# Performance work log

Measured on AMD Instinct MI355X. Metric: run time of the kernel, lower is better.

The kernel has to match this reference:

```python
import jax, jax.numpy as jnp
import numpy as np

BS, Q, NCLS, T = 16, 900, 1000, 100  # batch, queries, classes, targets per image
W_CLASS, W_BBOX, W_GIOU = 1.0, 1.0, 1.0


def _lsa_min(cost):
    """Jonker-Volgenant shortest-augmenting-path assignment (minimization).
    cost: [n, m] with n <= m. Returns (rows=arange(n), cols) matching
    scipy.optimize.linear_sum_assignment."""
    cost = np.asarray(cost, dtype=np.float64)
    n, m = cost.shape
    INF = np.inf
    u = np.zeros(n + 1)
    v = np.zeros(m + 1)
    p = np.zeros(m + 1, dtype=np.int64)   # p[j] = row (1-indexed) assigned to col j
    way = np.zeros(m + 1, dtype=np.int64)
    for i in range(1, n + 1):
        p[0] = i
        j0 = 0
        minv = np.full(m + 1, INF)
        used = np.zeros(m + 1, dtype=bool)
        while True:
            used[j0] = True
            i0 = p[j0]
            cur = cost[i0 - 1] - u[i0] - v[1:]
            free = ~used[1:]
            upd = free & (cur < minv[1:])
            minv[1:] = np.where(upd, cur, minv[1:])
            way[1:] = np.where(upd, j0, way[1:])
            free_idx = np.nonzero(free)[0]
            j1 = free_idx[np.argmin(minv[1:][free_idx])] + 1
            delta = minv[j1]
            used_idx = np.nonzero(used)[0]
            u[p[used_idx]] += delta
            v[used_idx] -= delta
            minv[1:][free] -= delta
            j0 = j1
            if p[j0] == 0:
                break
        while j0 != 0:
            j1 = way[j0]
            p[j0] = p[j1]
            j0 = j1
    cols = np.empty(n, dtype=np.int64)
    for j in range(1, m + 1):
        if p[j] > 0:
            cols[p[j] - 1] = j - 1
    return np.arange(n, dtype=np.int64), cols


def setup_inputs() -> dict:
    key = jax.random.key(0)
    k1, k2, k3, k4 = jax.random.split(key, 4)
    return {
        "pred_logits": jax.random.normal(k1, (BS, Q, NCLS), dtype=jnp.float32),
        "pred_boxes": jax.random.uniform(k2, (BS, Q, 4), dtype=jnp.float32),
        "tgt_ids": jax.random.randint(k3, (BS * T,), 0, NCLS, dtype=jnp.int64),
        "tgt_bbox": jax.random.uniform(k4, (BS * T, 4), dtype=jnp.float32),
    }


def _cost_matrix(pred_logits, pred_boxes, tgt_ids, tgt_bbox):
    out_prob = jax.nn.softmax(pred_logits.reshape(BS * Q, NCLS), axis=-1)
    out_bbox = pred_boxes.reshape(BS * Q, 4)
    cost_class = -out_prob[:, tgt_ids]                                   # [BS*Q, BS*T]
    cost_bbox = jnp.sum(jnp.abs(out_bbox[:, None, :] - tgt_bbox[None, :, :]), axis=-1)  # L1 cdist
    # cost_giou is zeros_like(cost_bbox) in the source, so its term vanishes
    Cm = W_BBOX * cost_bbox + W_CLASS * cost_class
    return Cm.reshape(BS, Q, BS * T)


def reference(pred_logits, pred_boxes, tgt_ids, tgt_bbox):
    Cm = _cost_matrix(pred_logits, pred_boxes, tgt_ids, tgt_bbox)
    Cnp = np.asarray(jax.device_get(Cm))
    idx_i, idx_j = [], []
    for b in range(BS):
        block = Cnp[b, :, b * T:(b + 1) * T]          # [Q, T], Q > T
        r, c = _lsa_min(block.T)                      # solve transpose: rows=targets, cols=preds
        order = np.argsort(c)                         # scipy sorts by prediction index
        idx_i.append(c[order])                        # selected prediction indices
        idx_j.append(r[order])                        # corresponding target indices
    return Cm, jnp.asarray(np.stack(idx_i)), jnp.asarray(np.stack(idx_j))
```

## Files before the change

### kernel.cpp

```cpp
#include <hip/hip_runtime.h>
#include <hip/hip_bf16.h>
#include <math.h>

#define BS   16
#define NQ   900
#define NCLS 1000
#define NT   100
#define MQ   900
#define NCOL (BS * NT)
#define NSLOT 15

typedef float f32x4 __attribute__((ext_vector_type(4)));

#define WAVE_FENCE() asm volatile("" ::: "memory")

__device__ __forceinline__ unsigned umin32(unsigned a, unsigned b) {
  return a < b ? a : b;
}

template <int CTRL>
__device__ __forceinline__ unsigned dpp_min_u32(unsigned x) {
  const unsigned o = (unsigned)__builtin_amdgcn_update_dpp(
      (int)x, (int)x, CTRL, 0xF, 0xF, false);
  return o < x ? o : x;
}

__device__ __forceinline__ unsigned wave_min_u32(unsigned x) {
  x = dpp_min_u32<0xB1>(x);
  x = dpp_min_u32<0x4E>(x);
  x = dpp_min_u32<0x114>(x);
  x = dpp_min_u32<0x118>(x);
  x = dpp_min_u32<0x142>(x);
  x = dpp_min_u32<0x143>(x);
  return (unsigned)__builtin_amdgcn_readlane((int)x, 63);
}

__device__ __forceinline__ unsigned f32key(float f) {
  unsigned e = __float_as_uint(f);
  return (e & 0x80000000u) ? ~e : (e | 0x80000000u);
}
__device__ __forceinline__ float f32unkey(unsigned k) {
  return __uint_as_float((k & 0x80000000u) ? (k ^ 0x80000000u) : ~k);
}

__global__ __launch_bounds__(256) void statcost_kernel(
    const float* __restrict__ logits, const float* __restrict__ boxes,
    const int* __restrict__ ids, const float* __restrict__ tbox,
    float* __restrict__ stats, float* __restrict__ costT, int id_stride) {
  const int tid = threadIdx.x, w = tid >> 6, lane = tid & 63;
  const int row = blockIdx.x * 4 + w;
  const int b = row / NQ;
  const int q = row - b * NQ;

  __shared__ float lbuf[4][NCLS];
  float* lr = lbuf[w];

  const float4* l4 = (const float4*)(logits + (size_t)row * NCLS);
  float4 vv[4];
  float lmax = -INFINITY;
#pragma unroll
  for (int it = 0; it < 4; ++it) {
    const int idx = it * 64 + lane;
    if (idx < NCLS / 4) {
      vv[it] = l4[idx];
      ((float4*)lr)[idx] = vv[it];
      lmax = fmaxf(lmax,
                   fmaxf(fmaxf(vv[it].x, vv[it].y), fmaxf(vv[it].z, vv[it].w)));
    }
  }
  for (int o = 32; o > 0; o >>= 1) lmax = fmaxf(lmax, __shfl_xor(lmax, o, 64));
  float psum = 0.f;
#pragma unroll
  for (int it = 0; it < 4; ++it) {
    const int idx = it * 64 + lane;
    if (idx < NCLS / 4) {
      psum += __expf(vv[it].x - lmax) + __expf(vv[it].y - lmax) +
              __expf(vv[it].z - lmax) + __expf(vv[it].w - lmax);
    }
  }
  for (int o = 32; o > 0; o >>= 1) psum += __shfl_xor(psum, o, 64);
  if (lane == 0) { stats[2 * row] = lmax; stats[2 * row + 1] = psum; }

  const float4 bb = *reinterpret_cast<const float4*>(boxes + (size_t)row * 4);
  const float inv = 1.f / psum;
  for (int rr = lane; rr < NT; rr += 64) {
    const int j = b * NT + rr;
    const int id = ids[(size_t)j * id_stride];
    const float4 tb = *reinterpret_cast<const float4*>(tbox + (size_t)j * 4);
    float d = fabsf(bb.x - tb.x);
    d += fabsf(bb.y - tb.y);
    d += fabsf(bb.z - tb.z);
    d += fabsf(bb.w - tb.w);
    costT[((size_t)b * NT + rr) * MQ + q] = d - __expf(lr[id] - lmax) * inv;
  }
}

__global__ __launch_bounds__(64) void rowmin_kernel(
    const float* __restrict__ costT, float* __restrict__ u_w,
    int* __restrict__ amin_w) {
  const int bid = blockIdx.x;
  const float* rowp = costT + (size_t)bid * MQ;
  const int lane = threadIdx.x;
  const unsigned UMAX = 0xFFFFFFFFu;

  unsigned tv[NSLOT];
#pragma unroll
  for (int s = 0; s < NSLOT; ++s) {
    const int c = s * 64 + lane;
    tv[s] = (c < MQ) ? f32key(rowp[c]) : UMAX;
  }
  unsigned m[NSLOT];
#pragma unroll
  for (int s = 0; s < NSLOT; ++s) m[s] = tv[s];
#pragma unroll
  for (int st = 1; st < NSLOT; st <<= 1) {
#pragma unroll
    for (int s = 0; s + st < NSLOT; s += 2 * st) m[s] = umin32(m[s], m[s + st]);
  }
  const unsigned s_vb = wave_min_u32(m[0]);
  unsigned cj[NSLOT];
#pragma unroll
  for (int s = 0; s < NSLOT; ++s)
    cj[s] = (tv[s] == s_vb) ? (unsigned)(s * 64 + lane) : UMAX;
#pragma unroll
  for (int st = 1; st < NSLOT; st <<= 1) {
#pragma unroll
    for (int s = 0; s + st < NSLOT; s += 2 * st)
      cj[s] = umin32(cj[s], cj[s + st]);
  }
  const unsigned s_j = wave_min_u32(cj[0]);
  if (lane == 0) { u_w[bid] = f32unkey(s_vb); amin_w[bid] = (int)s_j; }
}

__global__ __launch_bounds__(256) void main_kernel(
    const float* __restrict__ logits, const float* __restrict__ boxes,
    const int* __restrict__ ids, const float* __restrict__ tbox,
    const float* __restrict__ stats, const float* __restrict__ costT,
    const float* __restrict__ u_w, const int* __restrict__ amin_w,
    float* __restrict__ C, float* __restrict__ out_i,
    float* __restrict__ out_j, int id_stride) {
  __shared__ float lbuf[4][NCLS];
  __shared__ int p[MQ + 1];
  __shared__ int way[MQ + 65];
  __shared__ int cols[NT];
  __shared__ float warmbuf[256];

  if (blockIdx.x >= BS) {
    const int tid = threadIdx.x, w = tid >> 6, lane = tid & 63;
    const int row = (blockIdx.x - BS) * 4 + w;
    float* lr = lbuf[w];
    const f32x4* l4 = (const f32x4*)(logits + (size_t)row * NCLS);
#pragma unroll
    for (int it = 0; it < 4; ++it) {
      const int idx = it * 64 + lane;
      if (idx < NCLS / 4) {
        const f32x4 lv = __builtin_nontemporal_load(l4 + idx);
        ((f32x4*)lr)[idx] = lv;
      }
    }
    const float rmax = stats[2 * row];
    const float inv = 1.f / stats[2 * row + 1];
    const float4 bb = *reinterpret_cast<const float4*>(boxes + (size_t)row * 4);
    float* crow = C + (size_t)row * NCOL;
#pragma unroll
    for (int it = 0; it < 6; ++it) {
      const int c0 = it * 256 + lane * 4;
      int4 id4;
      if (id_stride == 1) {
        id4 = *reinterpret_cast<const int4*>(ids + c0);
      } else {
        const int4 a = *reinterpret_cast<const int4*>(ids + 2 * c0);
        const int4 bq = *reinterpret_cast<const int4*>(ids + 2 * c0 + 4);
        id4 = make_int4(a.x, a.z, bq.x, bq.z);
      }
      const float4 tb0 = *reinterpret_cast<const float4*>(tbox + (size_t)c0 * 4);
      const float4 tb1 =
          *reinterpret_cast<const float4*>(tbox + (size_t)(c0 + 1) * 4);
      const float4 tb2 =
          *reinterpret_cast<const float4*>(tbox + (size_t)(c0 + 2) * 4);
      const float4 tb3 =
          *reinterpret_cast<const float4*>(tbox + (size_t)(c0 + 3) * 4);
      f32x4 outv;
      {
        float d = fabsf(bb.x - tb0.x) + fabsf(bb.y - tb0.y) +
                  fabsf(bb.z - tb0.z) + fabsf(bb.w - tb0.w);
        outv.x = d - __expf(lr[id4.x] - rmax) * inv;
      }
      {
        float d = fabsf(bb.x - tb1.x) + fabsf(bb.y - tb1.y) +
                  fabsf(bb.z - tb1.z) + fabsf(bb.w - tb1.w);
        outv.y = d - __expf(lr[id4.y] - rmax) * inv;
      }
      {
        float d = fabsf(bb.x - tb2.x) + fabsf(bb.y - tb2.y) +
                  fabsf(bb.z - tb2.z) + fabsf(bb.w - tb2.w);
        outv.z = d - __expf(lr[id4.z] - rmax) * inv;
      }
      {
        float d = fabsf(bb.x - tb3.x) + fabsf(bb.y - tb3.y) +
                  fabsf(bb.z - tb3.z) + fabsf(bb.w - tb3.w);
        outv.w = d - __expf(lr[id4.w] - rmax) * inv;
      }
      __builtin_nontemporal_store(outv, reinterpret_cast<f32x4*>(crow + c0));
    }
    {
      const int c = 1536 + lane;
      const int id = ids[(size_t)c * id_stride];
      const float4 tb = *reinterpret_cast<const float4*>(tbox + (size_t)c * 4);
      float d = fabsf(bb.x - tb.x) + fabsf(bb.y - tb.y) + fabsf(bb.z - tb.z) +
                fabsf(bb.w - tb.w);
      __builtin_nontemporal_store(d - __expf(lr[id] - rmax) * inv, crow + c);
    }
    return;
  }

  if (threadIdx.x >= 64) return;
  const int b = blockIdx.x;
  const float* cost = costT + (size_t)b * NT * MQ;
  const int lane = threadIdx.x;
  const float FINF = __builtin_inff();
  const unsigned UMAX = 0xFFFFFFFFu;
  const unsigned UINFB = 0x7F800000u;

  float v[NSLOT];
  unsigned V32[NSLOT];
  float cfA[NSLOT], cfB[NSLOT];
  int jp[NSLOT];

#pragma unroll
  for (int s = 0; s < NSLOT; ++s) v[s] = 0.f;
  for (int j = lane; j <= MQ; j += 64) p[j] = 0;
  for (int r2 = lane; r2 < NT; r2 += 64) cols[r2] = -7777;
  WAVE_FENCE();

  float u0 = u_w[b * NT + lane];
  float u1 = (lane < NT - 64) ? u_w[b * NT + 64 + lane] : 0.f;
  const int a0 = amin_w[b * NT + lane];
  const int a1 = (lane < NT - 64) ? amin_w[b * NT + 64 + lane] : 0;

  for (int t = 0; t < 351; ++t) {
    __builtin_amdgcn_global_load_lds(
        (const __attribute__((address_space(1))) unsigned int*)
            (cost + t * 256 + lane * 4),
        (__attribute__((address_space(3))) unsigned int*)warmbuf, 16, 0, 0);
  }

  unsigned long long cl0 = 0, cl1 = 0;
  {
    unsigned clm = 0;
    for (int r2 = 0; r2 < NT; ++r2) {
      const int aj0 = (r2 < 64) ? __builtin_amdgcn_readlane(a0, r2)
                                : __builtin_amdgcn_readlane(a1, r2 - 64);
      const int slot = aj0 >> 6;
      const bool owner = (lane == (aj0 & 63));
      const unsigned long long bl = __ballot(owner && ((clm >> slot) & 1u));
      if (bl == 0) {
        if (owner) { clm |= 1u << slot; p[aj0 + 1] = r2 + 1; }
        if (r2 < 64) cl0 |= 1ull << r2;
        else         cl1 |= 1ull << (r2 - 64);
      }
    }
  }
  WAVE_FENCE();

#pragma unroll
  for (int s = 0; s < NSLOT; ++s) {
    const int c = s * 64 + lane;
    if (c < MQ) jp[s] = ((c + 1) << 7) | p[c + 1];
  }

  for (int i = 1; i <= NT; ++i) {
    const int r = i - 1;
    const bool skip = (r < 64) ? ((cl0 >> r) & 1ull) : ((cl1 >> (r - 64)) & 1ull);
    if (skip) continue;

    {
      const float* crow = cost + (size_t)r * MQ;
#pragma unroll
      for (int s = 0; s < NSLOT; ++s) {
        const int c = s * 64 + lane;
        cfA[s] = (c < MQ) ? crow[c] : FINF;
      }
    }
    float uir;
    {
      const float uu = (r < 64) ? u0 : u1;
      uir = __uint_as_float(
          (unsigned)__builtin_amdgcn_readlane((int)__float_as_uint(uu),
                                              r & 63));
    }

    unsigned usedm = (lane >= MQ - 14 * 64) ? (1u << 14) : 0u;
    int tm0 = 0, tm1 = 0;
    float D = 0.f;
#pragma unroll
    for (int s = 0; s < NSLOT; ++s) V32[s] = UINFB;
    if (lane == 0) p[0] = i;
    WAVE_FENCE();

    int j0 = 0;
    int i0 = i;
    float ui0 = uir;

    auto iterate = [&](float (&CUR)[NSLOT], float (&NXT)[NSLOT]) -> bool {
      if (j0 > 0) {
        const int cz = j0 - 1;
        const bool own = (lane == (cz & 63));
        usedm |= own ? (1u << (cz >> 6)) : 0u;
      }
      {
        const int ri = i0 - 1;
        tm0 |= (lane == ri) ? 1 : 0;
        tm1 |= (lane == (ri - 64)) ? 1 : 0;
      }

      const float a = ui0 - D;
      unsigned tv[NSLOT];
#pragma unroll
      for (int s = 0; s < NSLOT; ++s) {
        const bool us = (usedm >> s) & 1u;
        const float rel = fmaxf(CUR[s] - a - v[s], 0.f);
        const unsigned rb = __float_as_uint(rel);
        const unsigned rbg = us ? UMAX : rb;
        const bool upd = rbg < V32[s];
        way[upd ? (s * 64 + lane + 1) : 0] = j0;
        V32[s] = upd ? rbg : V32[s];
        tv[s] = us ? UMAX : V32[s];
      }
      unsigned m[NSLOT];
#pragma unroll
      for (int s = 0; s < NSLOT; ++s) m[s] = tv[s];
#pragma unroll
      for (int st = 1; st < NSLOT; st <<= 1) {
#pragma unroll
        for (int s = 0; s + st < NSLOT; s += 2 * st)
          m[s] = umin32(m[s], m[s + st]);
      }
      const unsigned s_best = wave_min_u32(m[0]);
      const float Dnew = __uint_as_float(s_best);

      unsigned cj[NSLOT];
#pragma unroll
      for (int s = 0; s < NSLOT; ++s)
        cj[s] = (tv[s] == s_best) ? (unsigned)jp[s] : UMAX;
#pragma unroll
      for (int st = 1; st < NSLOT; st <<= 1) {
#pragma unroll
        for (int s = 0; s + st < NSLOT; s += 2 * st)
          cj[s] = umin32(cj[s], cj[s + st]);
      }
      const unsigned jpw = wave_min_u32(cj[0]);
      const int j1 = (int)(jpw >> 7);
      const int pj1 = (int)(jpw & 127u);

      if (pj1 != 0) {
        const float* crow = cost + (size_t)(pj1 - 1) * MQ;
#pragma unroll
        for (int s = 0; s < NSLOT; ++s) {
          const int c = s * 64 + lane;
          NXT[s] = (c < MQ) ? crow[c] : FINF;
        }
      }
      float unext = 0.f;
      if (pj1 != 0) {
        const int rr2 = pj1 - 1;
        const float uu = (rr2 < 64) ? u0 : u1;
        unext = __uint_as_float(
            (unsigned)__builtin_amdgcn_readlane((int)__float_as_uint(uu),
                                                rr2 & 63));
      }

      const float delta = Dnew - D;
      D = Dnew;
      u0 += tm0 ? delta : 0.f;
      u1 += tm1 ? delta : 0.f;

      j0 = j1; i0 = pj1; ui0 = unext;
      return pj1 != 0;
    };

    while (true) {
      if (!iterate(cfA, cfB)) break;
      if (!iterate(cfB, cfA)) break;
    }

    {
      const float Dend = D;
#pragma unroll
      for (int s = 0; s < NSLOT; ++s) {
        const int c = s * 64 + lane;
        const bool us = (usedm >> s) & 1u;
        const float dv = __uint_as_float(V32[s]) - Dend;
        v[s] += (us && c < MQ) ? dv : 0.f;
      }
    }

    WAVE_FENCE();
    if (lane == 0) {
      int ja = j0;
      while (ja != 0) { const int jb = way[ja]; p[ja] = p[jb]; ja = jb; }
    }
    WAVE_FENCE();
#pragma unroll
    for (int s = 0; s < NSLOT; ++s) {
      const int c = s * 64 + lane;
      if (c < MQ) jp[s] = ((c + 1) << 7) | p[c + 1];
    }
  }

  WAVE_FENCE();
  for (int j = lane + 1; j <= MQ; j += 64)
    if (p[j] > 0) cols[p[j] - 1] = j - 1;
  WAVE_FENCE();

  for (int r = lane; r < NT; r += 64) {
    const int c = cols[r];
    int rank = 0;
    for (int r2 = 0; r2 < NT; ++r2) rank += (cols[r2] < c);
    out_i[b * NT + rank] = (float)c;
    out_j[b * NT + rank] = (float)r;
  }
}

extern "C" void kernel_launch(void* const* d_in, const int* in_sizes, int n_in,
                              void* d_out, int out_size, void* d_ws,
                              size_t ws_size, hipStream_t stream) {
  const float* logits = (const float*)d_in[0];
  const float* boxes  = (const float*)d_in[1];
  const int*   ids    = (const int*)d_in[2];
  const float* tbox   = (const float*)d_in[3];

  float* C     = (float*)d_out;
  float* out_i = C + (size_t)BS * NQ * NCOL;
  float* out_j = out_i + NCOL;

  float* costT = (float*)d_ws;
  float* stats = costT + (size_t)BS * NT * MQ;
  float* u_w   = stats + 2 * BS * NQ;
  int*   amin_w = (int*)(u_w + BS * NT);

  const int id_stride = (in_sizes[2] == 2 * NCOL) ? 2 : 1;

  statcost_kernel<<<BS * NQ / 4, 256, 0, stream>>>(logits, boxes, ids, tbox,
                                                   stats, costT, id_stride);
  rowmin_kernel<<<BS * NT, 64, 0, stream>>>(costT, u_w, amin_w);
  main_kernel<<<BS * NQ / 4 + BS, 256, 0, stream>>>(
      logits, boxes, ids, tbox, stats, costT, u_w, amin_w, C, out_i, out_j,
      id_stride);
}
```

Before: 88.27 us.

## Fuse row-min initialization into LSA blocks and drop separate rowmin kernel

Removes the standalone rowmin kernel launch and computes per-target row minima and argmins inside each batch's LSA block, using all four waves (25 rows each) with double-buffered register prefetch, storing results in shared memory. This also drops the global_load_lds cache-warming loop. It saves one kernel launch and the global round trip for u/amin. In exchange it puts the row-min scan on the critical path of the serial solver blocks and loses the explicit L2 warm-up of the cost block.

```diff
diff --git a/kernel.cpp b/kernel.cpp
--- a/kernel.cpp
+++ b/kernel.cpp
@@ -95,58 +95,24 @@
   }
 }
 
-__global__ __launch_bounds__(64) void rowmin_kernel(
-    const float* __restrict__ costT, float* __restrict__ u_w,
-    int* __restrict__ amin_w) {
-  const int bid = blockIdx.x;
-  const float* rowp = costT + (size_t)bid * MQ;
-  const int lane = threadIdx.x;
-  const unsigned UMAX = 0xFFFFFFFFu;
-
-  unsigned tv[NSLOT];
-#pragma unroll
-  for (int s = 0; s < NSLOT; ++s) {
-    const int c = s * 64 + lane;
-    tv[s] = (c < MQ) ? f32key(rowp[c]) : UMAX;
-  }
-  unsigned m[NSLOT];
-#pragma unroll
-  for (int s = 0; s < NSLOT; ++s) m[s] = tv[s];
-#pragma unroll
-  for (int st = 1; st < NSLOT; st <<= 1) {
-#pragma unroll
-    for (int s = 0; s + st < NSLOT; s += 2 * st) m[s] = umin32(m[s], m[s + st]);
-  }
-  const unsigned s_vb = wave_min_u32(m[0]);
-  unsigned cj[NSLOT];
-#pragma unroll
-  for (int s = 0; s < NSLOT; ++s)
-    cj[s] = (tv[s] == s_vb) ? (unsigned)(s * 64 + lane) : UMAX;
-#pragma unroll
-  for (int st = 1; st < NSLOT; st <<= 1) {
-#pragma unroll
-    for (int s = 0; s + st < NSLOT; s += 2 * st)
-      cj[s] = umin32(cj[s], cj[s + st]);
-  }
-  const unsigned s_j = wave_min_u32(cj[0]);
-  if (lane == 0) { u_w[bid] = f32unkey(s_vb); amin_w[bid] = (int)s_j; }
-}
-
 __global__ __launch_bounds__(256) void main_kernel(
     const float* __restrict__ logits, const float* __restrict__ boxes,
     const int* __restrict__ ids, const float* __restrict__ tbox,
     const float* __restrict__ stats, const float* __restrict__ costT,
-    const float* __restrict__ u_w, const int* __restrict__ amin_w,
     float* __restrict__ C, float* __restrict__ out_i,
     float* __restrict__ out_j, int id_stride) {
   __shared__ float lbuf[4][NCLS];
   __shared__ int p[MQ + 1];
   __shared__ int way[MQ + 65];
   __shared__ int cols[NT];
-  __shared__ float warmbuf[256];
+  __shared__ float u_s[NT];
+  __shared__ int amin_s[NT];
+
+  const int tid = threadIdx.x, w = tid >> 6, lane = tid & 63;
+  const float FINF = __builtin_inff();
+  const unsigned UMAX = 0xFFFFFFFFu;
 
   if (blockIdx.x >= BS) {
-    const int tid = threadIdx.x, w = tid >> 6, lane = tid & 63;
     const int row = (blockIdx.x - BS) * 4 + w;
     float* lr = lbuf[w];
     const f32x4* l4 = (const f32x4*)(logits + (size_t)row * NCLS);
@@ -214,14 +180,68 @@
     return;
   }
 
-  if (threadIdx.x >= 64) return;
   const int b = blockIdx.x;
   const float* cost = costT + (size_t)b * NT * MQ;
-  const int lane = threadIdx.x;
-  const float FINF = __builtin_inff();
-  const unsigned UMAX = 0xFFFFFFFFu;
+
+  {
+    float pfA[NSLOT], pfB[NSLOT];
+    const int r0 = w * 25;
+    {
+      const float* crow = cost + (size_t)r0 * MQ;
+#pragma unroll
+      for (int s = 0; s < NSLOT; ++s) {
+        const int c = s * 64 + lane;
+        pfA[s] = (c < MQ) ? crow[c] : FINF;
+      }
+    }
+    for (int k = 0; k < 25; ++k) {
+      if (k + 1 < 25) {
+        const float* crow = cost + (size_t)(r0 + k + 1) * MQ;
+#pragma unroll
+        for (int s = 0; s < NSLOT; ++s) {
+          const int c = s * 64 + lane;
+          pfB[s] = (c < MQ) ? crow[c] : FINF;
+        }
+      }
+      unsigned tv[NSLOT];
+#pragma unroll
+      for (int s = 0; s < NSLOT; ++s) {
+        const int c = s * 64 + lane;
+        tv[s] = (c < MQ) ? f32key(pfA[s]) : UMAX;
+      }
+      unsigned m[NSLOT];
+#pragma unroll
+      for (int s = 0; s < NSLOT; ++s) m[s] = tv[s];
+#pragma unroll
+      for (int st = 1; st < NSLOT; st <<= 1) {
+#pragma unroll
+        for (int s = 0; s + st < NSLOT; s += 2 * st)
+          m[s] = umin32(m[s], m[s + st]);
+      }
+      const unsigned s_vb = wave_min_u32(m[0]);
+      unsigned cj[NSLOT];
+#pragma unroll
+      for (int s = 0; s < NSLOT; ++s)
+        cj[s] = (tv[s] == s_vb) ? (unsigned)(s * 64 + lane) : UMAX;
+#pragma unroll
+      for (int st = 1; st < NSLOT; st <<= 1) {
+#pragma unroll
+        for (int s = 0; s + st < NSLOT; s += 2 * st)
+          cj[s] = umin32(cj[s], cj[s + st]);
+      }
+      const unsigned s_j = wave_min_u32(cj[0]);
+      if (lane == 0) {
+        u_s[r0 + k] = f32unkey(s_vb);
+        amin_s[r0 + k] = (int)s_j;
+      }
+#pragma unroll
+      for (int s = 0; s < NSLOT; ++s) pfA[s] = pfB[s];
+    }
+  }
+  __syncthreads();
+  if (tid >= 64) return;
+
   const unsigned UINFB = 0x7F800000u;
-
   float v[NSLOT];
   unsigned V32[NSLOT];
   float cfA[NSLOT], cfB[NSLOT];
@@ -233,17 +253,10 @@
   for (int r2 = lane; r2 < NT; r2 += 64) cols[r2] = -7777;
   WAVE_FENCE();
 
-  float u0 = u_w[b * NT + lane];
-  float u1 = (lane < NT - 64) ? u_w[b * NT + 64 + lane] : 0.f;
-  const int a0 = amin_w[b * NT + lane];
-  const int a1 = (lane < NT - 64) ? amin_w[b * NT + 64 + lane] : 0;
-
-  for (int t = 0; t < 351; ++t) {
-    __builtin_amdgcn_global_load_lds(
-        (const __attribute__((address_space(1))) unsigned int*)
-            (cost + t * 256 + lane * 4),
-        (__attribute__((address_space(3))) unsigned int*)warmbuf, 16, 0, 0);
-  }
+  float u0 = u_s[lane];
+  float u1 = (lane < NT - 64) ? u_s[64 + lane] : 0.f;
+  const int a0 = amin_s[lane];
+  const int a1 = (lane < NT - 64) ? amin_s[64 + lane] : 0;
 
   unsigned long long cl0 = 0, cl1 = 0;
   {
@@ -436,15 +449,11 @@
 
   float* costT = (float*)d_ws;
   float* stats = costT + (size_t)BS * NT * MQ;
-  float* u_w   = stats + 2 * BS * NQ;
-  int*   amin_w = (int*)(u_w + BS * NT);
 
   const int id_stride = (in_sizes[2] == 2 * NCOL) ? 2 : 1;
 
   statcost_kernel<<<BS * NQ / 4, 256, 0, stream>>>(logits, boxes, ids, tbox,
                                                    stats, costT, id_stride);
-  rowmin_kernel<<<BS * NT, 64, 0, stream>>>(costT, u_w, amin_w);
   main_kernel<<<BS * NQ / 4 + BS, 256, 0, stream>>>(
-      logits, boxes, ids, tbox, stats, costT, u_w, amin_w, C, out_i, out_j,
-      id_stride);
-}
+      logits, boxes, ids, tbox, stats, costT, C, out_i, out_j, id_stride);
+}
```

New measurement: 94.54 us. 7.1% more time.
